# Performance work log

Measured on AMD Instinct MI355X. Metric: run time of the kernel, lower is better.

The kernel has to match this reference:

```python
import jax, jax.numpy as jnp
import numpy as np

S = 8192        # packed patch tokens
D = 1024        # hidden_size
H = 16          # num_heads
DH = D // H     # head_dim = 64
N_SEG = 8       # images
SEG = S // N_SEG


def _rope_tables(seq_len, dim, theta=10000.0):
    inv_freq = 1.0 / (theta ** (jnp.arange(0, dim, 2, dtype=jnp.float32) / dim))
    pos = jnp.arange(seq_len, dtype=jnp.float32)
    freqs = pos[:, None] * inv_freq[None, :]          # [S, dim//2]
    emb = jnp.concatenate([freqs, freqs], axis=-1)    # [S, dim]
    return jnp.cos(emb), jnp.sin(emb)


def setup_inputs() -> dict:
    key = jax.random.key(0)
    ks = jax.random.split(key, 6)
    hidden_states = jax.random.normal(ks[0], (S, D), dtype=jnp.float32)
    cu_seqlens = (jnp.arange(N_SEG + 1, dtype=jnp.int32) * SEG)
    cos, sin = _rope_tables(S, DH)
    scale = 1.0 / np.sqrt(D)
    qkv_w = jax.random.normal(ks[1], (3 * D, D), dtype=jnp.float32) * scale
    qkv_b = jax.random.normal(ks[2], (3 * D,), dtype=jnp.float32) * 0.02
    proj_w = jax.random.normal(ks[3], (D, D), dtype=jnp.float32) * scale
    proj_b = jax.random.normal(ks[4], (D,), dtype=jnp.float32) * 0.02
    return {"hidden_states": hidden_states, "cos": cos, "sin": sin,
            "qkv_w": qkv_w, "qkv_b": qkv_b, "proj_w": proj_w, "proj_b": proj_b,
            "cu_seqlens": cu_seqlens}


def _rotate_half(x):
    x1, x2 = jnp.split(x, 2, axis=-1)
    return jnp.concatenate([-x2, x1], axis=-1)


def reference(hidden_states, cos, sin, qkv_w, qkv_b, proj_w, proj_b, cu_seqlens):
    seq = hidden_states.shape[0]
    n_seg = cu_seqlens.shape[0] - 1
    seg = seq // n_seg  # equal-length packed segments

    qkv = hidden_states @ qkv_w.T + qkv_b                # [S, 3D]
    qkv = qkv.reshape(seq, 3, H, DH)
    q, k, v = qkv[:, 0], qkv[:, 1], qkv[:, 2]            # [S, H, DH]

    # rotary in fp32, cos/sin broadcast over heads (unsqueeze(-2))
    cosf = cos[:, None, :].astype(jnp.float32)
    sinf = sin[:, None, :].astype(jnp.float32)
    qf = q.astype(jnp.float32)
    kf = k.astype(jnp.float32)
    q = (qf * cosf + _rotate_half(qf) * sinf).astype(q.dtype)
    k = (kf * cosf + _rotate_half(kf) * sinf).astype(k.dtype)

    # block-diagonal attention over cu_seqlens segments (all equal length)
    qb = q.reshape(n_seg, seg, H, DH)
    kb = k.reshape(n_seg, seg, H, DH)
    vb = v.reshape(n_seg, seg, H, DH)
    scaling = DH ** -0.5
    scores = jnp.einsum('nqhd,nkhd->nhqk', qb, kb) * scaling
    probs = jax.nn.softmax(scores.astype(jnp.float32), axis=-1).astype(qb.dtype)
    out = jnp.einsum('nhqk,nkhd->nqhd', probs, vb)       # [n, seg, H, DH]
    out = out.reshape(seq, D)

    return out @ proj_w.T + proj_b
```

## Files before the change

### kernel.cpp

```cpp
#include <hip/hip_runtime.h>
#include <hip/hip_bf16.h>
#include <cstdint>
#include <cstddef>

typedef __bf16 bf16_t;
typedef __bf16 bf16x4 __attribute__((ext_vector_type(4)));
typedef __bf16 bf16x8 __attribute__((ext_vector_type(8)));
typedef float  f32x4  __attribute__((ext_vector_type(4)));

#define S_LEN 8192
#define NHEAD 16
#define DHEAD 64
#define NSEG  8
#define SEG   1024

#define QSCALE 0.1803368801111204f

__device__ __forceinline__ void stage16(const void* gsrc, void* lds_base, int lane) {
#if __has_builtin(__builtin_amdgcn_global_load_lds)
  (void)lane;
  __builtin_amdgcn_global_load_lds(
      (__attribute__((address_space(1))) void*)(gsrc),
      (__attribute__((address_space(3))) void*)(lds_base), 16, 0, 0);
#else
  ((uint4*)lds_base)[lane] = *(const uint4*)gsrc;
#endif
}

__global__ __launch_bounds__(256) void cvt_all_kernel(
    const float* __restrict__ s0, bf16_t* __restrict__ d0,
    const float* __restrict__ s1, bf16_t* __restrict__ d1,
    const float* __restrict__ s2, bf16_t* __restrict__ d2) {
  int b = blockIdx.x;
  const float* src;
  bf16_t* dst;
  int i;
  if (b < 8192)      { src = s0; dst = d0; i = b * 256 + threadIdx.x; }
  else if (b < 11264){ src = s1; dst = d1; i = (b - 8192) * 256 + threadIdx.x; }
  else               { src = s2; dst = d2; i = (b - 11264) * 256 + threadIdx.x; }
  float4 f = ((const float4*)src)[i];
  bf16x4 o = {(bf16_t)f.x, (bf16_t)f.y, (bf16_t)f.z, (bf16_t)f.w};
  ((bf16x4*)dst)[i] = o;
}

template<int MODE, int N, int K>
__global__ __launch_bounds__(256, 2) void gemm_bt_kernel(
    const bf16_t* __restrict__ A, const bf16_t* __restrict__ B,
    const float* __restrict__ bias, void* __restrict__ Cout,
    bf16_t* __restrict__ vt, const float* __restrict__ cosT,
    const float* __restrict__ sinT) {
  __shared__ __align__(16) bf16_t As[2][128 * 32];
  __shared__ __align__(16) bf16_t Bs[2][128 * 32];
  const int tid = threadIdx.x;
  const int wv = tid >> 6, lane = tid & 63;
  const int quad = lane >> 4, l16 = lane & 15;
  const int m0 = blockIdx.y * 128, n0 = blockIdx.x * 128;
  const int wm = (wv >> 1) * 64, wn = (wv & 1) * 64;

  const int c0 = wv * 2, c1 = wv * 2 + 1;
  const int rr = lane & 15;
  const int kc = (lane >> 4) * 8;
  const bf16_t* Ap0 = A + (size_t)(m0 + c0 * 16 + rr) * K + kc;
  const bf16_t* Ap1 = A + (size_t)(m0 + c1 * 16 + rr) * K + kc;
  const bf16_t* Bp0 = B + (size_t)(n0 + c0 * 16 + rr) * K + kc;
  const bf16_t* Bp1 = B + (size_t)(n0 + c1 * 16 + rr) * K + kc;

  f32x4 acc[4][4];
#pragma unroll
  for (int i = 0; i < 4; i++)
#pragma unroll
    for (int j = 0; j < 4; j++) {
      f32x4 z = {0.f, 0.f, 0.f, 0.f};
      acc[i][j] = z;
    }

  constexpr int NK = K / 32;
  stage16(Ap0, &As[0][c0 * 512], lane);
  stage16(Ap1, &As[0][c1 * 512], lane);
  stage16(Bp0, &Bs[0][c0 * 512], lane);
  stage16(Bp1, &Bs[0][c1 * 512], lane);

  for (int kbi = 0; kbi < NK; kbi++) {
    __syncthreads();
    if (kbi + 1 < NK) {
      const int kb = (kbi + 1) * 32;
      bf16_t* ad = As[(kbi + 1) & 1];
      bf16_t* bd = Bs[(kbi + 1) & 1];
      stage16(Ap0 + kb, ad + c0 * 512, lane);
      stage16(Ap1 + kb, ad + c1 * 512, lane);
      stage16(Bp0 + kb, bd + c0 * 512, lane);
      stage16(Bp1 + kb, bd + c1 * 512, lane);
    }
    const bf16_t* as = As[kbi & 1];
    const bf16_t* bs = Bs[kbi & 1];
    bf16x8 af[4], bfr[4];
#pragma unroll
    for (int i = 0; i < 4; i++)
      af[i] = *(const bf16x8*)&as[wm * 32 + i * 512 + quad * 128 + l16 * 8];
#pragma unroll
    for (int j = 0; j < 4; j++)
      bfr[j] = *(const bf16x8*)&bs[wn * 32 + j * 512 + quad * 128 + l16 * 8];
#pragma unroll
    for (int i = 0; i < 4; i++)
#pragma unroll
      for (int j = 0; j < 4; j++)
        acc[i][j] = __builtin_amdgcn_mfma_f32_16x16x32_bf16(af[i], bfr[j], acc[i][j], 0, 0, 0);
  }

#pragma unroll
  for (int i = 0; i < 4; i++) {
    const int row = m0 + wm + i * 16 + quad * 4;
#pragma unroll
    for (int j = 0; j < 4; j++) {
      const int col = n0 + wn + j * 16 + l16;
      if (MODE == 0) {
        if (col < 2048) {
          if (j < 2) {
            bf16_t* qkp = (bf16_t*)Cout;
            const int d = col & 63;
            const float bv0 = bias[col];
            const float bv1 = bias[col + 32];
            const bool isq = (col < 1024);
            const int cb0 = (col >> 3) & 7;
            const int cb1 = cb0 + 4;
            const size_t base = (size_t)(col & ~63);
#pragma unroll
            for (int r = 0; r < 4; r++) {
              const int s = row + r;
              const float c = cosT[s * 64 + d];
              const float sn = sinT[s * 64 + d];
              const float x1 = acc[i][j][r] + bv0;
              const float x2 = acc[i][j + 2][r] + bv1;
              float o1 = x1 * c - x2 * sn;
              float o2 = x2 * c + x1 * sn;
              if (isq) { o1 *= QSCALE; o2 *= QSCALE; }
              const int sw = s & 7;
              const size_t rb = (size_t)s * 2048 + base + (col & 7);
              qkp[rb + ((cb0 ^ sw) * 8)] = (bf16_t)o1;
              qkp[rb + ((cb1 ^ sw) * 8)] = (bf16_t)o2;
            }
          }
        } else {
          const float bv = bias[col];
          const int h = (col - 2048) >> 6, d = (col - 2048) & 63;
          const int seg = row >> 10, kl0 = row & 1023;
          const int blk = (((kl0 & 63) >> 3) ^ (d & 7));
          bf16x4 pk = {(bf16_t)(acc[i][j][0] + bv), (bf16_t)(acc[i][j][1] + bv),
                       (bf16_t)(acc[i][j][2] + bv), (bf16_t)(acc[i][j][3] + bv)};
          *(bf16x4*)&vt[((size_t)((seg * NHEAD + h) * DHEAD + d)) * SEG +
                        (kl0 & ~63) + blk * 8 + (kl0 & 7)] = pk;
        }
      } else {
        const float bv = bias[col];
        float* cp = (float*)Cout;
#pragma unroll
        for (int r = 0; r < 4; r++)
          cp[(size_t)(row + r) * N + col] = acc[i][j][r] + bv;
      }
    }
  }
}

__global__ __launch_bounds__(256, 2) void attn_kernel(
    const bf16_t* __restrict__ qk, const bf16_t* __restrict__ vt,
    bf16_t* __restrict__ attn) {
  __shared__ __align__(16) bf16_t Qs[64 * 64];
  __shared__ __align__(16) bf16_t Ks[2][64 * 64];
  __shared__ __align__(16) bf16_t Vs[2][64 * 64];
  __shared__ __align__(16) bf16_t Ps[4][16 * 64];

  const int bid = blockIdx.x;
  const int qt = bid & 15;
  const int h = (bid >> 4) & 15;
  const int seg = bid >> 8;
  const int tid = threadIdx.x;
  const int wv = tid >> 6, lane = tid & 63;
  const int quad = lane >> 4, l16 = lane & 15;
  const int swl = l16 & 7;

  const int c0 = wv * 2, c1 = c0 + 1;
  const int r8 = lane >> 3;
  const int k8 = (lane & 7) * 8;

  const bf16_t* kbase = qk + 1024 + h * 64;
  const bf16_t* vbase = vt + (size_t)((seg * NHEAD + h) * DHEAD) * SEG;

  {
    size_t rowbase = (size_t)(seg * SEG + qt * 64);
    stage16(qk + (rowbase + c0 * 8 + r8) * 2048 + h * 64 + k8, &Qs[c0 * 512], lane);
    stage16(qk + (rowbase + c1 * 8 + r8) * 2048 + h * 64 + k8, &Qs[c1 * 512], lane);
    size_t krow = (size_t)(seg * SEG);
    stage16(kbase + (krow + c0 * 8 + r8) * 2048 + k8, &Ks[0][c0 * 512], lane);
    stage16(kbase + (krow + c1 * 8 + r8) * 2048 + k8, &Ks[0][c1 * 512], lane);
    stage16(vbase + (size_t)(c0 * 8 + r8) * SEG + k8, &Vs[0][c0 * 512], lane);
    stage16(vbase + (size_t)(c1 * 8 + r8) * SEG + k8, &Vs[0][c1 * 512], lane);
  }
  __syncthreads();
  const bf16x8 aq0 = *(const bf16x8*)&Qs[(wv * 16 + l16) * 64 + (quad ^ swl) * 8];
  const bf16x8 aq1 = *(const bf16x8*)&Qs[(wv * 16 + l16) * 64 + ((quad + 4) ^ swl) * 8];

  float rs[4] = {0.f, 0.f, 0.f, 0.f};
  f32x4 o[4];
#pragma unroll
  for (int jd = 0; jd < 4; jd++) { f32x4 z = {0.f, 0.f, 0.f, 0.f}; o[jd] = z; }

  for (int kt = 0; kt < 16; kt++) {
    __syncthreads();
    if (kt + 1 < 16) {
      const int nb = (kt + 1) & 1;
      size_t krow = (size_t)(seg * SEG + (kt + 1) * 64);
      stage16(kbase + (krow + c0 * 8 + r8) * 2048 + k8, &Ks[nb][c0 * 512], lane);
      stage16(kbase + (krow + c1 * 8 + r8) * 2048 + k8, &Ks[nb][c1 * 512], lane);
      stage16(vbase + (size_t)(c0 * 8 + r8) * SEG + (kt + 1) * 64 + k8, &Vs[nb][c0 * 512], lane);
      stage16(vbase + (size_t)(c1 * 8 + r8) * SEG + (kt + 1) * 64 + k8, &Vs[nb][c1 * 512], lane);
    }
    const bf16_t* ks = Ks[kt & 1];
    const bf16_t* vs = Vs[kt & 1];

    f32x4 sacc[4];
#pragma unroll
    for (int j = 0; j < 4; j++) {
      bf16x8 b0 = *(const bf16x8*)&ks[(j * 16 + l16) * 64 + (quad ^ swl) * 8];
      bf16x8 b1 = *(const bf16x8*)&ks[(j * 16 + l16) * 64 + ((quad + 4) ^ swl) * 8];
      f32x4 s = {0.f, 0.f, 0.f, 0.f};
      s = __builtin_amdgcn_mfma_f32_16x16x32_bf16(aq0, b0, s, 0, 0, 0);
      s = __builtin_amdgcn_mfma_f32_16x16x32_bf16(aq1, b1, s, 0, 0, 0);
      sacc[j] = s;
    }

#pragma unroll
    for (int j = 0; j < 4; j++)
#pragma unroll
      for (int r = 0; r < 4; r++) {
        float e = exp2f(sacc[j][r]);
        rs[r] += e;
        const int prow = quad * 4 + r;
        const int pblk = (j * 2 + (l16 >> 3)) ^ (prow & 7);
        Ps[wv][prow * 64 + pblk * 8 + (l16 & 7)] = (bf16_t)e;
      }

    bf16x8 ap0 = *(const bf16x8*)&Ps[wv][l16 * 64 + (quad ^ swl) * 8];
    bf16x8 ap1 = *(const bf16x8*)&Ps[wv][l16 * 64 + ((quad + 4) ^ swl) * 8];
#pragma unroll
    for (int jd = 0; jd < 4; jd++) {
      bf16x8 b0 = *(const bf16x8*)&vs[(jd * 16 + l16) * 64 + (quad ^ swl) * 8];
      bf16x8 b1 = *(const bf16x8*)&vs[(jd * 16 + l16) * 64 + ((quad + 4) ^ swl) * 8];
      o[jd] = __builtin_amdgcn_mfma_f32_16x16x32_bf16(ap0, b0, o[jd], 0, 0, 0);
      o[jd] = __builtin_amdgcn_mfma_f32_16x16x32_bf16(ap1, b1, o[jd], 0, 0, 0);
    }
  }

#pragma unroll
  for (int r = 0; r < 4; r++) {
#pragma unroll
    for (int off = 1; off < 16; off <<= 1) rs[r] += __shfl_xor(rs[r], off);
    rs[r] = 1.0f / rs[r];
  }

  const int srow = seg * SEG + qt * 64 + wv * 16 + quad * 4;
#pragma unroll
  for (int jd = 0; jd < 4; jd++) {
    const int col = h * 64 + jd * 16 + l16;
#pragma unroll
    for (int r = 0; r < 4; r++)
      attn[(size_t)(srow + r) * 1024 + col] = (bf16_t)(o[jd][r] * rs[r]);
  }
}

extern "C" void kernel_launch(void* const* d_in, const int* in_sizes, int n_in,
                              void* d_out, int out_size, void* d_ws, size_t ws_size,
                              hipStream_t stream) {
  const float* hidden = (const float*)d_in[0];
  const float* cosT   = (const float*)d_in[1];
  const float* sinT   = (const float*)d_in[2];
  const float* qkv_w  = (const float*)d_in[3];
  const float* qkv_b  = (const float*)d_in[4];
  const float* proj_w = (const float*)d_in[5];
  const float* proj_b = (const float*)d_in[6];

  char* ws = (char*)d_ws;
  bf16_t* hs   = (bf16_t*)(ws);
  bf16_t* qw   = (bf16_t*)(ws + 16777216);
  bf16_t* pw   = (bf16_t*)(ws + 23068672);
  bf16_t* qkb  = (bf16_t*)(ws + 25165824);
  bf16_t* vtb  = (bf16_t*)(ws + 58720256);
  bf16_t* attb = (bf16_t*)(ws + 75497472);
  float* out = (float*)d_out;

  cvt_all_kernel<<<12288, 256, 0, stream>>>(hidden, hs, qkv_w, qw, proj_w, pw);

  gemm_bt_kernel<0, 3072, 1024><<<dim3(24, 64), 256, 0, stream>>>(
      hs, qw, qkv_b, (void*)qkb, vtb, cosT, sinT);
  attn_kernel<<<2048, 256, 0, stream>>>(qkb, vtb, attb);
  gemm_bt_kernel<1, 1024, 1024><<<dim3(8, 64), 256, 0, stream>>>(
      attb, pw, proj_b, (void*)out, nullptr, nullptr, nullptr);
}
```

Baseline: 319.2 us.

## Pre-tile GEMM operands into MFMA-fragment layout for contiguous LDS staging

```diff
diff --git a/kernel.cpp b/kernel.cpp
--- a/kernel.cpp
+++ b/kernel.cpp
@@ -27,20 +27,34 @@
 #endif
 }
 
-__global__ __launch_bounds__(256) void cvt_all_kernel(
+__global__ __launch_bounds__(256) void cvt_tile_kernel(
     const float* __restrict__ s0, bf16_t* __restrict__ d0,
     const float* __restrict__ s1, bf16_t* __restrict__ d1,
     const float* __restrict__ s2, bf16_t* __restrict__ d2) {
+  __shared__ __align__(16) bf16_t T[16 * 1024];
   int b = blockIdx.x;
-  const float* src;
-  bf16_t* dst;
-  int i;
-  if (b < 8192)      { src = s0; dst = d0; i = b * 256 + threadIdx.x; }
-  else if (b < 11264){ src = s1; dst = d1; i = (b - 8192) * 256 + threadIdx.x; }
-  else               { src = s2; dst = d2; i = (b - 11264) * 256 + threadIdx.x; }
-  float4 f = ((const float4*)src)[i];
-  bf16x4 o = {(bf16_t)f.x, (bf16_t)f.y, (bf16_t)f.z, (bf16_t)f.w};
-  ((bf16x4*)dst)[i] = o;
+  const float* src; bf16_t* dst; int rb;
+  if (b < 512)      { src = s0; dst = d0; rb = b; }
+  else if (b < 704) { src = s1; dst = d1; rb = b - 512; }
+  else              { src = s2; dst = d2; rb = b - 704; }
+  const int t = threadIdx.x;
+  const size_t base4 = (size_t)rb * 4096;
+#pragma unroll
+  for (int i = 0; i < 16; i++) {
+    int f = i * 256 + t;
+    float4 v = ((const float4*)src)[base4 + f];
+    bf16x4 o = {(bf16_t)v.x, (bf16_t)v.y, (bf16_t)v.z, (bf16_t)v.w};
+    *(bf16x4*)&T[f * 4] = o;
+  }
+  __syncthreads();
+  bf16_t* dt = dst + (size_t)rb * 16384;
+#pragma unroll
+  for (int i = 0; i < 8; i++) {
+    int o = i * 2048 + t * 8;
+    int tile = o >> 9, kb = (o >> 7) & 3, r = (o >> 3) & 15;
+    bf16x8 v = *(const bf16x8*)&T[r * 1024 + tile * 32 + kb * 8];
+    *(bf16x8*)&dt[o] = v;
+  }
 }
 
 template<int MODE, int N, int K>
@@ -57,13 +71,12 @@
   const int m0 = blockIdx.y * 128, n0 = blockIdx.x * 128;
   const int wm = (wv >> 1) * 64, wn = (wv & 1) * 64;
 
+  constexpr int KT = K / 32;
   const int c0 = wv * 2, c1 = wv * 2 + 1;
-  const int rr = lane & 15;
-  const int kc = (lane >> 4) * 8;
-  const bf16_t* Ap0 = A + (size_t)(m0 + c0 * 16 + rr) * K + kc;
-  const bf16_t* Ap1 = A + (size_t)(m0 + c1 * 16 + rr) * K + kc;
-  const bf16_t* Bp0 = B + (size_t)(n0 + c0 * 16 + rr) * K + kc;
-  const bf16_t* Bp1 = B + (size_t)(n0 + c1 * 16 + rr) * K + kc;
+  const bf16_t* Ap0 = A + ((size_t)((m0 >> 4) + c0) * KT) * 512 + lane * 8;
+  const bf16_t* Ap1 = A + ((size_t)((m0 >> 4) + c1) * KT) * 512 + lane * 8;
+  const bf16_t* Bp0 = B + ((size_t)((n0 >> 4) + c0) * KT) * 512 + lane * 8;
+  const bf16_t* Bp1 = B + ((size_t)((n0 >> 4) + c1) * KT) * 512 + lane * 8;
 
   f32x4 acc[4][4];
 #pragma unroll
@@ -74,16 +87,15 @@
       acc[i][j] = z;
     }
 
-  constexpr int NK = K / 32;
   stage16(Ap0, &As[0][c0 * 512], lane);
   stage16(Ap1, &As[0][c1 * 512], lane);
   stage16(Bp0, &Bs[0][c0 * 512], lane);
   stage16(Bp1, &Bs[0][c1 * 512], lane);
 
-  for (int kbi = 0; kbi < NK; kbi++) {
+  for (int kbi = 0; kbi < KT; kbi++) {
     __syncthreads();
-    if (kbi + 1 < NK) {
-      const int kb = (kbi + 1) * 32;
+    if (kbi + 1 < KT) {
+      const int kb = (kbi + 1) * 512;
       bf16_t* ad = As[(kbi + 1) & 1];
       bf16_t* bd = Bs[(kbi + 1) & 1];
       stage16(Ap0 + kb, ad + c0 * 512, lane);
@@ -96,10 +108,10 @@
     bf16x8 af[4], bfr[4];
 #pragma unroll
     for (int i = 0; i < 4; i++)
-      af[i] = *(const bf16x8*)&as[wm * 32 + i * 512 + quad * 128 + l16 * 8];
+      af[i] = *(const bf16x8*)&as[((wm >> 4) + i) * 512 + lane * 8];
 #pragma unroll
     for (int j = 0; j < 4; j++)
-      bfr[j] = *(const bf16x8*)&bs[wn * 32 + j * 512 + quad * 128 + l16 * 8];
+      bfr[j] = *(const bf16x8*)&bs[((wn >> 4) + j) * 512 + lane * 8];
 #pragma unroll
     for (int i = 0; i < 4; i++)
 #pragma unroll
@@ -257,13 +269,17 @@
     rs[r] = 1.0f / rs[r];
   }
 
-  const int srow = seg * SEG + qt * 64 + wv * 16 + quad * 4;
-#pragma unroll
-  for (int jd = 0; jd < 4; jd++) {
-    const int col = h * 64 + jd * 16 + l16;
-#pragma unroll
-    for (int r = 0; r < 4; r++)
-      attn[(size_t)(srow + r) * 1024 + col] = (bf16_t)(o[jd][r] * rs[r]);
+  {
+    bf16_t* abase = attn + (size_t)(seg * 64 + qt * 4 + wv) * 16384;
+#pragma unroll
+    for (int jd = 0; jd < 4; jd++) {
+      const int ct = h * 2 + (jd >> 1);
+      const int kb = (jd & 1) * 2 + (l16 >> 3);
+      const int e = l16 & 7;
+#pragma unroll
+      for (int r = 0; r < 4; r++)
+        abase[ct * 512 + kb * 128 + (quad * 4 + r) * 8 + e] = (bf16_t)(o[jd][r] * rs[r]);
+    }
   }
 }
 
@@ -287,7 +303,7 @@
   bf16_t* attb = (bf16_t*)(ws + 75497472);
   float* out = (float*)d_out;
 
-  cvt_all_kernel<<<12288, 256, 0, stream>>>(hidden, hs, qkv_w, qw, proj_w, pw);
+  cvt_tile_kernel<<<768, 256, 0, stream>>>(hidden, hs, qkv_w, qw, proj_w, pw);
 
   gemm_bt_kernel<0, 3072, 1024><<<dim3(24, 64), 256, 0, stream>>>(
       hs, qw, qkv_b, (void*)qkb, vtb, cosT, sinT);
```

New measurement: 272.2 us. 1.17x faster.
